# Optimization experiments

Hardware: AMD Instinct MI355X
Metric: run time of the kernel (lower is better)

Reference implementation:

```python
import jax, jax.numpy as jnp
import numpy as np
from jax import lax

PI = 3.14159265
# (dh, dw) for each of the 8 discretized angle bins, matching the torch `direction` table
DIRS = jnp.array([[1, 0], [1, 1], [0, 1], [-1, 1], [-1, 0], [-1, -1], [0, -1], [1, -1]], dtype=jnp.int32)
CC_ITERS = 48  # fixed trip count; FastSV converges in O(log N) rounds (log2(512*512)=18)


def _grids(H, W):
    return jnp.meshgrid(jnp.arange(H, dtype=jnp.int32), jnp.arange(W, dtype=jnp.int32), indexing='ij')


def _find_parents(angles, theta_a):
    # vectorized version of find_parents: per-pixel angle bin -> neighbor; root if OOB or angle gap too large
    H, W = angles.shape
    ii, jj = _grids(H, W)
    pos = jnp.round((angles + PI / 8.0) / (PI / 4.0))
    pos = jnp.where(pos >= 8.0, pos - 8.0, pos).astype(jnp.int32)
    nh = ii + DIRS[pos, 0]
    nw = jj + DIRS[pos, 1]
    inb = (nh >= 0) & (nh < H) & (nw >= 0) & (nw < W)
    nhc = jnp.clip(nh, 0, H - 1)
    nwc = jnp.clip(nw, 0, W - 1)
    ad = jnp.abs(angles - angles[nhc, nwc])
    ad = jnp.minimum(ad, 2.0 * PI - ad)
    is_root = (~inb) | (ad > theta_a * PI / 180.0)
    ph = jnp.where(is_root, ii, nhc)
    pw = jnp.where(is_root, jj, nwc)
    return ph, pw, is_root


def _cc_min_label(u, v, n):
    # Parallel union-find with min-label semantics (FastSV: root hooking + pointer jumping).
    # Equivalent to the serial UNION/FIND: final label of each pixel = min pixel index in its component.
    f0 = jnp.arange(n, dtype=jnp.int32)

    def body(_, f):
        fu, fv = f[u], f[v]
        m = jnp.minimum(fu, fv)
        g = f.at[fu].min(m).at[fv].min(m).at[u].min(m).at[v].min(m)
        g = g[g]
        g = g[g]
        return g

    return lax.fori_loop(0, CC_ITERS, body, f0)


def _structures(angles, theta_a):
    # All integer / discrete structure: parents, union-find labels, 3-step ancestors, boundary masks.
    H, W = angles.shape
    N = H * W
    ii, jj = _grids(H, W)
    ph, pw, roots = _find_parents(angles, theta_a)
    pf = (ph * W + pw).reshape(-1)  # flat parent pointer per pixel
    idx = jnp.arange(N, dtype=jnp.int32)
    # stage-1 edges: pixel <-> parent; stage-2 edges: merge_nearby_root_pixels window
    # range(0, min(3, H-1-i)) x range(-min(3, j), min(3, W-1-j))  <=>  dh in {0,1,2} with nh<=H-2,
    # dw in {-3..2} with 0<=nw<=W-2, both endpoints roots
    us, vs = [idx], [pf]
    for dh in range(0, 3):
        for dw in range(-3, 3):
            nh, nw = ii + dh, jj + dw
            nhc = jnp.clip(nh, 0, H - 1)
            nwc = jnp.clip(nw, 0, W - 1)
            m = roots & (nh <= H - 2) & (nw >= 0) & (nw <= W - 2) & roots[nhc, nwc]
            us.append(jnp.where(m, ii * W + jj, 0).reshape(-1))
            vs.append(jnp.where(m, nhc * W + nwc, 0).reshape(-1))
    labels_after = _cc_min_label(jnp.concatenate(us), jnp.concatenate(vs), N) + 1  # super_BPDs after dilation
    c3 = pf[pf[pf]]  # 3-step parent chase for every pixel (as in find_bnd_angle_diff)
    # boundary masks for right (0,1) and down (1,0) neighbors
    masks, nidxs = [], []
    for dh, dw in ((0, 1), (1, 0)):
        nh, nw = ii + dh, jj + dw
        valid = ((nh < H) & (nw < W)).reshape(-1)
        nidx = (jnp.clip(nh, 0, H - 1) * W + jnp.clip(nw, 0, W - 1)).reshape(-1)
        masks.append(valid & (labels_after != labels_after[nidx]))
        nidxs.append(nidx)
    return c3, masks, nidxs


def _bnd_angle_diff(angles, c3, masks, nidxs):
    # per boundary pixel-pair: wrap-around angle difference of the two 3-step ancestors
    H, W = angles.shape
    ang = angles.reshape(-1)
    outs = []
    for mask, nidx in zip(masks, nidxs):
        ad = jnp.abs(ang[c3] - ang[c3[nidx]])
        ad = jnp.minimum(ad, 2.0 * PI - ad)
        outs.append(jnp.where(mask, ad, 0.0))
    return jnp.stack(outs, axis=-1).reshape(H, W, 2)


def setup_inputs():
    key = jax.random.key(0)
    H, W = 512, 512
    input_angles = jax.random.uniform(key, (H, W), jnp.float32, 0.0, 2.0 * PI)
    return {"input_angles": input_angles, "height": H, "width": W, "theta_a": 45, "S_o": 90}


def reference(input_angles, height, width, theta_a, S_o):
    c3, masks, nidxs = _structures(input_angles, theta_a)
    return _bnd_angle_diff(input_angles, c3, masks, nidxs)
```

## Files before the change

### kernel.cpp

```cpp
#include <hip/hip_runtime.h>


static constexpr double PI_D = 3.14159265;

__device__ __constant__ int c_DH[8] = {1, 1, 0, -1, -1, -1, 0, 1};
__device__ __constant__ int c_DW[8] = {0, 1, 1, 1, 0, -1, -1, -1};

__device__ int g_fb[3 * 262144];

__device__ __forceinline__ int uf_find_lds(int x, int* par) {
    while (true) {
        int p = par[x];
        if (p == x) return x;
        int gp = par[p];
        if (gp == p) return p;
        atomicMin(&par[x], gp);
        x = gp;
    }
}
__device__ __forceinline__ void uf_unite_lds(int u, int v, int* par) {
    int ru = uf_find_lds(u, par);
    int rv = uf_find_lds(v, par);
    while (ru != rv) {
        if (ru > rv) { int t2 = ru; ru = rv; rv = t2; }
        int old = atomicMin(&par[rv], ru);
        if (old == rv) break;
        rv = uf_find_lds(old, par);
        ru = uf_find_lds(ru, par);
    }
}

__device__ __forceinline__ int find_ro(int x, const int* par) {
    int p = par[x];
    while (p != x) { x = p; p = par[x]; }
    return x;
}
__device__ __forceinline__ void uf_unite(int u, int v, int* par) {
    int ru = find_ro(u, par);
    int rv = find_ro(v, par);
    while (ru != rv) {
        if (ru > rv) { int t2 = ru; ru = rv; rv = t2; }
        int old = atomicMin(&par[rv], ru);
        if (old == rv) break;
        rv = find_ro(old, par);
        ru = find_ro(ru, par);
    }
}

__device__ __forceinline__ bool parent_dir(const float* __restrict__ ang, float a,
                                           int i, int j, int H, int W, float thr,
                                           int& nhc, int& nwc) {
    const float a8 = (float)(PI_D / 8.0);
    const float a4 = (float)(PI_D / 4.0);
    float posf = rintf((a + a8) / a4);
    if (posf >= 8.0f) posf -= 8.0f;
    const int pos = (int)posf;
    const int nh = i + c_DH[pos];
    const int nw = j + c_DW[pos];
    const bool inb = (nh >= 0) & (nh < H) & (nw >= 0) & (nw < W);
    nhc = min(max(nh, 0), H - 1);
    nwc = min(max(nw, 0), W - 1);
    float ad = fabsf(a - ang[nhc * W + nwc]);
    const float twopi = (float)(2.0 * PI_D);
    ad = fminf(ad, twopi - ad);
    return (!inb) || (ad > thr);
}

__global__ void __launch_bounds__(1024)
k_local(const float* __restrict__ ang,
        const int* __restrict__ hp, const int* __restrict__ wp,
        const int* __restrict__ tap, int N,
        int* __restrict__ pf, int* __restrict__ par, int* __restrict__ c3) {
    const int H = hp[0], W = wp[0];
    const float thr = (float)((double)tap[0] * PI_D / 180.0);
    const int tpr = (W + 31) >> 5;
    const int ntiles = tpr * ((H + 31) >> 5);
    __shared__ int lpar[1024];
    __shared__ int lpl[1024];
    const int lp = threadIdx.x;
    const int li = lp >> 5, lj = lp & 31;
    for (int tile = blockIdx.x; tile < ntiles; tile += gridDim.x) {
        const int ti0 = (tile / tpr) << 5, tj0 = (tile % tpr) << 5;
        const int i = ti0 + li, j = tj0 + lj;
        const bool inpix = (i < H) && (j < W);
        const int g = i * W + j;
        lpar[lp] = lp;
        int lparent = lp;
        if (inpix) {
            int nh, nw;
            const bool root = parent_dir(ang, ang[g], i, j, H, W, thr, nh, nw);
            pf[g] = root ? g : (nh * W + nw);
            if (!root) {
                const int pli = nh - ti0, plj = nw - tj0;
                lparent = (((unsigned)pli < 32u) && ((unsigned)plj < 32u))
                              ? ((pli << 5) + plj) : -1;
            }
        }
        lpl[lp] = lparent;
        __syncthreads();
        if (inpix) {
            if (lparent != lp) {
                if (lparent >= 0) uf_unite_lds(lp, lparent, lpar);
            } else if (i <= H - 2) {
                for (int d = 1; d <= 3; ++d) {
                    if (lj + d > 31 || j + d > W - 1) break;
                    if (lpl[lp + d] == lp + d) { uf_unite_lds(lp, lp + d, lpar); break; }
                }
                for (int dh = 1; dh <= 2; ++dh) {
                    const int nh = i + dh;
                    if (nh > H - 2) break;
                    const int nli = li + dh;
                    if (nli >= 32) break;
                    int first = -1, last = -1;
                    for (int dw = -3; dw <= 2; ++dw) {
                        const int nw = j + dw;
                        if ((unsigned)nw > (unsigned)(W - 2)) continue;
                        const int nlj = lj + dw;
                        if ((unsigned)nlj > 31u) continue;
                        const int nlp = (nli << 5) + nlj;
                        if (lpl[nlp] == nlp) { if (first < 0) first = nlp; last = nlp; }
                    }
                    if (first >= 0) {
                        uf_unite_lds(lp, first, lpar);
                        if (last != first) uf_unite_lds(lp, last, lpar);
                    }
                }
            }
        }
        __syncthreads();
        if (inpix) {
            const int lr = uf_find_lds(lp, lpar);
            par[g] = (ti0 + (lr >> 5)) * W + (tj0 + (lr & 31));
            if (li >= 3 && li <= 28 && lj >= 3 && lj <= 28) {
                int v = lpl[lp];
                v = lpl[v];
                v = lpl[v];
                c3[g] = (ti0 + (v >> 5)) * W + (tj0 + (v & 31));
            }
        }
        __syncthreads();
    }
}

__global__ void k_edges(const int* __restrict__ pf,
                        const int* __restrict__ hp, const int* __restrict__ wp,
                        int N, int* par) {
    const int H = hp[0], W = wp[0];
    const int tpr = (W + 31) >> 5;
    const int ntiles = tpr * ((H + 31) >> 5);
    const int tidx = threadIdx.x;
    __shared__ unsigned long long htab[256];
    int li = 0, lj = 0;
    if (tidx < 96) {
        const int r = tidx >> 5;
        li = (r == 0) ? 0 : 29 + r;
        lj = tidx & 31;
    } else if (tidx < 270) {
        const int u = tidx - 96;
        li = 1 + u / 6;
        const int c = u % 6;
        lj = (c < 3) ? c : 26 + c;
    }
    for (int tile = blockIdx.x; tile < ntiles; tile += gridDim.x) {
        for (int s = tidx; s < 256; s += blockDim.x) htab[s] = ~0ull;
        __syncthreads();
        const int i = ((tile / tpr) << 5) + li;
        const int j = ((tile % tpr) << 5) + lj;
        if (tidx < 270 && i < H && j < W) {
            const int t = i * W + j;
            auto EMIT = [&](int a, int b) {
                if (a == b) return;
                const int lo = min(a, b), hi2 = max(a, b);
                const unsigned long long key =
                    ((unsigned long long)lo << 20) | (unsigned)hi2;
                unsigned h = (unsigned)((key * 0x9E3779B97F4A7C15ull) >> 52) & 255u;
                bool fresh = true;
                for (int pr = 0; pr < 16; ++pr) {
                    unsigned long long old = atomicCAS(&htab[h], ~0ull, key);
                    if (old == ~0ull) break;
                    if (old == key) { fresh = false; break; }
                    h = (h + 1) & 255u;
                }
                if (fresh) uf_unite(lo, hi2, par);
            };
            const int p = pf[t];
            if (p != t) {
                const int pi = p / W, pj = p - pi * W;
                if (((pi ^ i) | (pj ^ j)) & ~31) EMIT(par[t], par[p]);
            } else if (i <= H - 2) {
                const int pt = par[t];
                int h0 = -1, h1 = -1;
                for (int d = (lj >= 29 ? 32 - lj : 4); d <= 3; ++d) {
                    if (j + d > W - 1) break;
                    const int n = t + d;
                    if (pf[n] != n) continue;
                    const int pn = par[n];
                    if (pn == pt || pn == h0 || pn == h1) continue;
                    h1 = h0; h0 = pn;
                    EMIT(pt, pn);
                }
                for (int dh = 1; dh <= 2; ++dh) {
                    const int nh = i + dh;
                    if (nh > H - 2) break;
                    const bool rowcross = (li + dh) > 31;
                    for (int dw = -3; dw <= 2; ++dw) {
                        const int nw = j + dw;
                        if ((unsigned)nw > (unsigned)(W - 2)) continue;
                        if (!rowcross && ((unsigned)(lj + dw) <= 31u)) continue;
                        const int n = nh * W + nw;
                        if (pf[n] != n) continue;
                        const int pn = par[n];
                        if (pn == pt || pn == h0 || pn == h1) continue;
                        h1 = h0; h0 = pn;
                        EMIT(pt, pn);
                    }
                }
            }
        }
        __syncthreads();
    }
}

__global__ void __launch_bounds__(256)
k_output(const float* __restrict__ ang,
         const int* __restrict__ par, const int* __restrict__ pf,
         const int* __restrict__ c3,
         const int* __restrict__ hp, const int* __restrict__ wp,
         float* __restrict__ out) {
    const int H = hp[0], W = wp[0];
    const int i0 = blockIdx.y << 3;
    const int j0 = blockIdx.x << 5;
    __shared__ int lab[9][33];
    const int tid = threadIdx.x;
    for (int k = tid; k < 9 * 33; k += 256) {
        const int r = k / 33, c = k - r * 33;
        const int gi = min(i0 + r, H - 1), gj = min(j0 + c, W - 1);
        lab[r][c] = find_ro(gi * W + gj, par);
    }
    __syncthreads();
    const int li2 = tid >> 5, lj2 = tid & 31;
    const int i = i0 + li2, j = j0 + lj2;
    if (i >= H || j >= W) return;
    const int t = i * W + j;
    const float twopi = (float)(2.0 * PI_D);
    const int l = lab[li2][lj2];
    float r0 = 0.0f, r1 = 0.0f;
    bool need = false;
    int l1 = l, l2 = l;
    if (j + 1 < W) { l1 = lab[li2][lj2 + 1]; need |= (l1 != l); }
    if (i + 1 < H) { l2 = lab[li2 + 1][lj2]; need |= (l2 != l); }
    if (need) {
        auto c3v = [&](int x, int xli, int xlj) {
            if (xli >= 3 && xli <= 28 && xlj >= 3 && xlj <= 28) return c3[x];
            int p = pf[x];
            p = pf[p];
            return pf[p];
        };
        const float ac = ang[c3v(t, i & 31, j & 31)];
        if (l1 != l) {
            float ad = fabsf(ac - ang[c3v(t + 1, i & 31, (j + 1) & 31)]);
            r0 = fminf(ad, twopi - ad);
        }
        if (l2 != l) {
            float ad = fabsf(ac - ang[c3v(t + W, (i + 1) & 31, j & 31)]);
            r1 = fminf(ad, twopi - ad);
        }
    }
    reinterpret_cast<float2*>(out)[t] = make_float2(r0, r1);
}

extern "C" void kernel_launch(void* const* d_in, const int* in_sizes, int n_in,
                              void* d_out, int out_size, void* d_ws, size_t ws_size,
                              hipStream_t stream) {
    const float* ang = (const float*)d_in[0];
    const int* hp  = (const int*)d_in[1];
    const int* wp  = (const int*)d_in[2];
    const int* tap = (const int*)d_in[3];
    const int N = in_sizes[0];

    int* base = (int*)d_ws;
    if (ws_size < (size_t)3 * (size_t)N * sizeof(int) && N <= 262144) {
        void* p = nullptr;
        hipGetSymbolAddress(&p, HIP_SYMBOL(g_fb));
        base = (int*)p;
    }
    int* pf  = base;
    int* par = base + N;
    int* c3  = base + 2 * N;

    k_local<<<256, 1024, 0, stream>>>(ang, hp, wp, tap, N, pf, par, c3);
    k_edges<<<256, 320, 0, stream>>>(pf, hp, wp, N, par);
    {
        const int H = 512, W = 512;
        dim3 gridO((W + 31) / 32, (H + 7) / 8);
        k_output<<<gridO, 256, 0, stream>>>(ang, par, pf, c3, hp, wp, (float*)d_out);
    }
}
```

Before: 97.19 us.

## Fuse three kernels into one cooperative kernel with grid-wide syncs

Merges the local labeling, boundary-edge union and output kernels into a single cooperative kernel of 256 blocks by 1024 threads, separated by grid.sync barriers. The output phase now runs over 32x32 tiles with a 33x33 label buffer in shared memory instead of 32x8 tiles. The aim is to remove the kernel launch gaps between the three stages. In exchange it adds grid-barrier cost, runs the edge phase with 1024-thread blocks where most threads idle, and depends on all 256 blocks being co-resident.

```diff
diff --git a/kernel.cpp b/kernel.cpp
--- a/kernel.cpp
+++ b/kernel.cpp
@@ -1,7 +1,12 @@
 #include <hip/hip_runtime.h>
+#include <hip/hip_cooperative_groups.h>
+
+namespace cg = cooperative_groups;
 
 
 static constexpr double PI_D = 3.14159265;
+#define NB 256
+#define NT 1024
 
 __device__ __constant__ int c_DH[8] = {1, 1, 0, -1, -1, -1, 0, 1};
 __device__ __constant__ int c_DW[8] = {0, 1, 1, 1, 0, -1, -1, -1};
@@ -66,19 +71,23 @@
     return (!inb) || (ad > thr);
 }
 
-__global__ void __launch_bounds__(1024)
-k_local(const float* __restrict__ ang,
-        const int* __restrict__ hp, const int* __restrict__ wp,
-        const int* __restrict__ tap, int N,
-        int* __restrict__ pf, int* __restrict__ par, int* __restrict__ c3) {
+__global__ void __launch_bounds__(NT, 1)
+k_all(const float* __restrict__ ang,
+      const int* __restrict__ hp, const int* __restrict__ wp,
+      const int* __restrict__ tap, int N,
+      int* __restrict__ pf, int* par, int* __restrict__ c3,
+      float* __restrict__ out) {
     const int H = hp[0], W = wp[0];
     const float thr = (float)((double)tap[0] * PI_D / 180.0);
     const int tpr = (W + 31) >> 5;
     const int ntiles = tpr * ((H + 31) >> 5);
     __shared__ int lpar[1024];
     __shared__ int lpl[1024];
+    __shared__ unsigned long long htab[256];
+    __shared__ int lab[33][33];
     const int lp = threadIdx.x;
     const int li = lp >> 5, lj = lp & 31;
+
     for (int tile = blockIdx.x; tile < ntiles; tile += gridDim.x) {
         const int ti0 = (tile / tpr) << 5, tj0 = (tile % tpr) << 5;
         const int i = ti0 + li, j = tj0 + lj;
@@ -140,133 +149,121 @@
         }
         __syncthreads();
     }
-}
-
-__global__ void k_edges(const int* __restrict__ pf,
-                        const int* __restrict__ hp, const int* __restrict__ wp,
-                        int N, int* par) {
-    const int H = hp[0], W = wp[0];
-    const int tpr = (W + 31) >> 5;
-    const int ntiles = tpr * ((H + 31) >> 5);
-    const int tidx = threadIdx.x;
-    __shared__ unsigned long long htab[256];
-    int li = 0, lj = 0;
-    if (tidx < 96) {
-        const int r = tidx >> 5;
-        li = (r == 0) ? 0 : 29 + r;
-        lj = tidx & 31;
-    } else if (tidx < 270) {
-        const int u = tidx - 96;
-        li = 1 + u / 6;
-        const int c = u % 6;
-        lj = (c < 3) ? c : 26 + c;
-    }
-    for (int tile = blockIdx.x; tile < ntiles; tile += gridDim.x) {
-        for (int s = tidx; s < 256; s += blockDim.x) htab[s] = ~0ull;
-        __syncthreads();
-        const int i = ((tile / tpr) << 5) + li;
-        const int j = ((tile % tpr) << 5) + lj;
-        if (tidx < 270 && i < H && j < W) {
-            const int t = i * W + j;
-            auto EMIT = [&](int a, int b) {
-                if (a == b) return;
-                const int lo = min(a, b), hi2 = max(a, b);
-                const unsigned long long key =
-                    ((unsigned long long)lo << 20) | (unsigned)hi2;
-                unsigned h = (unsigned)((key * 0x9E3779B97F4A7C15ull) >> 52) & 255u;
-                bool fresh = true;
-                for (int pr = 0; pr < 16; ++pr) {
-                    unsigned long long old = atomicCAS(&htab[h], ~0ull, key);
-                    if (old == ~0ull) break;
-                    if (old == key) { fresh = false; break; }
-                    h = (h + 1) & 255u;
-                }
-                if (fresh) uf_unite(lo, hi2, par);
-            };
-            const int p = pf[t];
-            if (p != t) {
-                const int pi = p / W, pj = p - pi * W;
-                if (((pi ^ i) | (pj ^ j)) & ~31) EMIT(par[t], par[p]);
-            } else if (i <= H - 2) {
-                const int pt = par[t];
-                int h0 = -1, h1 = -1;
-                for (int d = (lj >= 29 ? 32 - lj : 4); d <= 3; ++d) {
-                    if (j + d > W - 1) break;
-                    const int n = t + d;
-                    if (pf[n] != n) continue;
-                    const int pn = par[n];
-                    if (pn == pt || pn == h0 || pn == h1) continue;
-                    h1 = h0; h0 = pn;
-                    EMIT(pt, pn);
-                }
-                for (int dh = 1; dh <= 2; ++dh) {
-                    const int nh = i + dh;
-                    if (nh > H - 2) break;
-                    const bool rowcross = (li + dh) > 31;
-                    for (int dw = -3; dw <= 2; ++dw) {
-                        const int nw = j + dw;
-                        if ((unsigned)nw > (unsigned)(W - 2)) continue;
-                        if (!rowcross && ((unsigned)(lj + dw) <= 31u)) continue;
-                        const int n = nh * W + nw;
+    cg::this_grid().sync();
+
+    {
+        int bi = 0, bj = 0;
+        const int tidx = lp;
+        if (tidx < 96) {
+            const int r = tidx >> 5;
+            bi = (r == 0) ? 0 : 29 + r;
+            bj = tidx & 31;
+        } else if (tidx < 270) {
+            const int u = tidx - 96;
+            bi = 1 + u / 6;
+            const int c = u % 6;
+            bj = (c < 3) ? c : 26 + c;
+        }
+        for (int tile = blockIdx.x; tile < ntiles; tile += gridDim.x) {
+            for (int s = tidx; s < 256; s += NT) htab[s] = ~0ull;
+            __syncthreads();
+            const int i = ((tile / tpr) << 5) + bi;
+            const int j = ((tile % tpr) << 5) + bj;
+            if (tidx < 270 && i < H && j < W) {
+                const int t = i * W + j;
+                auto EMIT = [&](int a, int b) {
+                    if (a == b) return;
+                    const int lo = min(a, b), hi2 = max(a, b);
+                    const unsigned long long key =
+                        ((unsigned long long)lo << 20) | (unsigned)hi2;
+                    unsigned h = (unsigned)((key * 0x9E3779B97F4A7C15ull) >> 52) & 255u;
+                    bool fresh = true;
+                    for (int pr = 0; pr < 16; ++pr) {
+                        unsigned long long old = atomicCAS(&htab[h], ~0ull, key);
+                        if (old == ~0ull) break;
+                        if (old == key) { fresh = false; break; }
+                        h = (h + 1) & 255u;
+                    }
+                    if (fresh) uf_unite(lo, hi2, par);
+                };
+                const int p = pf[t];
+                if (p != t) {
+                    const int pi = p / W, pj = p - pi * W;
+                    if (((pi ^ i) | (pj ^ j)) & ~31) EMIT(par[t], par[p]);
+                } else if (i <= H - 2) {
+                    const int pt = par[t];
+                    int h0 = -1, h1 = -1;
+                    for (int d = (bj >= 29 ? 32 - bj : 4); d <= 3; ++d) {
+                        if (j + d > W - 1) break;
+                        const int n = t + d;
                         if (pf[n] != n) continue;
                         const int pn = par[n];
                         if (pn == pt || pn == h0 || pn == h1) continue;
                         h1 = h0; h0 = pn;
                         EMIT(pt, pn);
                     }
-                }
-            }
-        }
-        __syncthreads();
-    }
-}
-
-__global__ void __launch_bounds__(256)
-k_output(const float* __restrict__ ang,
-         const int* __restrict__ par, const int* __restrict__ pf,
-         const int* __restrict__ c3,
-         const int* __restrict__ hp, const int* __restrict__ wp,
-         float* __restrict__ out) {
-    const int H = hp[0], W = wp[0];
-    const int i0 = blockIdx.y << 3;
-    const int j0 = blockIdx.x << 5;
-    __shared__ int lab[9][33];
-    const int tid = threadIdx.x;
-    for (int k = tid; k < 9 * 33; k += 256) {
-        const int r = k / 33, c = k - r * 33;
-        const int gi = min(i0 + r, H - 1), gj = min(j0 + c, W - 1);
-        lab[r][c] = find_ro(gi * W + gj, par);
-    }
-    __syncthreads();
-    const int li2 = tid >> 5, lj2 = tid & 31;
-    const int i = i0 + li2, j = j0 + lj2;
-    if (i >= H || j >= W) return;
-    const int t = i * W + j;
+                    for (int dh = 1; dh <= 2; ++dh) {
+                        const int nh = i + dh;
+                        if (nh > H - 2) break;
+                        const bool rowcross = (bi + dh) > 31;
+                        for (int dw = -3; dw <= 2; ++dw) {
+                            const int nw = j + dw;
+                            if ((unsigned)nw > (unsigned)(W - 2)) continue;
+                            if (!rowcross && ((unsigned)(bj + dw) <= 31u)) continue;
+                            const int n = nh * W + nw;
+                            if (pf[n] != n) continue;
+                            const int pn = par[n];
+                            if (pn == pt || pn == h0 || pn == h1) continue;
+                            h1 = h0; h0 = pn;
+                            EMIT(pt, pn);
+                        }
+                    }
+                }
+            }
+            __syncthreads();
+        }
+    }
+    cg::this_grid().sync();
+
     const float twopi = (float)(2.0 * PI_D);
-    const int l = lab[li2][lj2];
-    float r0 = 0.0f, r1 = 0.0f;
-    bool need = false;
-    int l1 = l, l2 = l;
-    if (j + 1 < W) { l1 = lab[li2][lj2 + 1]; need |= (l1 != l); }
-    if (i + 1 < H) { l2 = lab[li2 + 1][lj2]; need |= (l2 != l); }
-    if (need) {
-        auto c3v = [&](int x, int xli, int xlj) {
-            if (xli >= 3 && xli <= 28 && xlj >= 3 && xlj <= 28) return c3[x];
-            int p = pf[x];
-            p = pf[p];
-            return pf[p];
-        };
-        const float ac = ang[c3v(t, i & 31, j & 31)];
-        if (l1 != l) {
-            float ad = fabsf(ac - ang[c3v(t + 1, i & 31, (j + 1) & 31)]);
-            r0 = fminf(ad, twopi - ad);
-        }
-        if (l2 != l) {
-            float ad = fabsf(ac - ang[c3v(t + W, (i + 1) & 31, j & 31)]);
-            r1 = fminf(ad, twopi - ad);
-        }
-    }
-    reinterpret_cast<float2*>(out)[t] = make_float2(r0, r1);
+    for (int tile = blockIdx.x; tile < ntiles; tile += gridDim.x) {
+        const int ti0 = (tile / tpr) << 5, tj0 = (tile % tpr) << 5;
+        for (int k = lp; k < 33 * 33; k += NT) {
+            const int r = k / 33, c = k - r * 33;
+            const int gi = min(ti0 + r, H - 1), gj = min(tj0 + c, W - 1);
+            lab[r][c] = find_ro(gi * W + gj, par);
+        }
+        __syncthreads();
+        const int i = ti0 + li, j = tj0 + lj;
+        if (i < H && j < W) {
+            const int t = i * W + j;
+            const int l = lab[li][lj];
+            float r0 = 0.0f, r1 = 0.0f;
+            bool need = false;
+            int l1 = l, l2 = l;
+            if (j + 1 < W) { l1 = lab[li][lj + 1]; need |= (l1 != l); }
+            if (i + 1 < H) { l2 = lab[li + 1][lj]; need |= (l2 != l); }
+            if (need) {
+                auto c3v = [&](int x, int xli, int xlj) {
+                    if (xli >= 3 && xli <= 28 && xlj >= 3 && xlj <= 28) return c3[x];
+                    int p = pf[x];
+                    p = pf[p];
+                    return pf[p];
+                };
+                const float ac = ang[c3v(t, li, lj)];
+                if (l1 != l) {
+                    float ad = fabsf(ac - ang[c3v(t + 1, li, (j + 1) & 31)]);
+                    r0 = fminf(ad, twopi - ad);
+                }
+                if (l2 != l) {
+                    float ad = fabsf(ac - ang[c3v(t + W, (i + 1) & 31, lj)]);
+                    r1 = fminf(ad, twopi - ad);
+                }
+            }
+            reinterpret_cast<float2*>(out)[t] = make_float2(r0, r1);
+        }
+        __syncthreads();
+    }
 }
 
 extern "C" void kernel_launch(void* const* d_in, const int* in_sizes, int n_in,
@@ -276,7 +273,7 @@
     const int* hp  = (const int*)d_in[1];
     const int* wp  = (const int*)d_in[2];
     const int* tap = (const int*)d_in[3];
-    const int N = in_sizes[0];
+    int N = in_sizes[0];
 
     int* base = (int*)d_ws;
     if (ws_size < (size_t)3 * (size_t)N * sizeof(int) && N <= 262144) {
@@ -287,12 +284,9 @@
     int* pf  = base;
     int* par = base + N;
     int* c3  = base + 2 * N;
-
-    k_local<<<256, 1024, 0, stream>>>(ang, hp, wp, tap, N, pf, par, c3);
-    k_edges<<<256, 320, 0, stream>>>(pf, hp, wp, N, par);
-    {
-        const int H = 512, W = 512;
-        dim3 gridO((W + 31) / 32, (H + 7) / 8);
-        k_output<<<gridO, 256, 0, stream>>>(ang, par, pf, c3, hp, wp, (float*)d_out);
-    }
-}
+    float* op = (float*)d_out;
+
+    void* kargs[] = {(void*)&ang, (void*)&hp, (void*)&wp, (void*)&tap,
+                     (void*)&N, (void*)&pf, (void*)&par, (void*)&c3, (void*)&op};
+    hipLaunchCooperativeKernel((const void*)k_all, dim3(NB), dim3(NT), kargs, 0, stream);
+}
```

Result: slower. 161.6 us (+66.3%).
